# Optimization experiments

Measured on AMD Instinct MI355X. Metric: run time of the kernel, lower is better.

## Reference

```python
import math
import jax, jax.numpy as jnp
import numpy as np

B = 128          # batch_size (graphs)
SEQ = 128        # max_seq_len (nodes per graph)
D = 128          # input_dim
HID = 64         # enc_hidden_dim
HEADS = 4        # in_head
N = B * SEQ      # total nodes
E = 262144       # edges (avg degree 16)


def _make_pe(seq, d):
    pos = np.arange(seq, dtype=np.float32)[:, None]
    i_even = np.arange(0, d, 2, dtype=np.float32)
    pe = np.zeros((seq, d), dtype=np.float32)
    pe[:, 0::2] = np.sin(pos / 10000.0 ** (2.0 * i_even / d))
    pe[:, 1::2] = np.cos(pos / 10000.0 ** (2.0 * (i_even + 1.0) / d))
    return jnp.asarray(pe)


def setup_inputs() -> dict:
    key = jax.random.key(0)
    ks = jax.random.split(key, 10)
    s = 0.1
    return {
        "x": jax.random.normal(ks[0], (N, D), jnp.float32),
        "edge_index": jax.random.randint(ks[1], (2, E), 0, N),
        "pe": _make_pe(SEQ, D),
        "W1": jax.random.normal(ks[2], (D, HEADS * HID), jnp.float32) * s,
        "a_src1": jax.random.normal(ks[3], (HEADS, HID), jnp.float32) * s,
        "a_dst1": jax.random.normal(ks[4], (HEADS, HID), jnp.float32) * s,
        "b1": jnp.zeros((HEADS * HID,), jnp.float32),
        "W2": jax.random.normal(ks[5], (HEADS * HID, HID), jnp.float32) * s,
        "a_src2": jax.random.normal(ks[6], (1, HID), jnp.float32) * s,
        "a_dst2": jax.random.normal(ks[7], (1, HID), jnp.float32) * s,
        "b2": jnp.zeros((HID,), jnp.float32),
        "batch_size": B,
    }


def _gat_conv(x, src, dst, W, a_src, a_dst, b, heads, ch, concat, n):
    # PyG GATConv (eval mode, self-loops already appended to src/dst).
    h = (x @ W).reshape(n, heads, ch)                      # [N,H,C]
    alpha_src = jnp.einsum("nhc,hc->nh", h, a_src)         # [N,H]
    alpha_dst = jnp.einsum("nhc,hc->nh", h, a_dst)
    e = jax.nn.leaky_relu(alpha_src[src] + alpha_dst[dst], 0.2)  # [E,H]
    m = jax.ops.segment_max(e, dst, num_segments=n)        # segment softmax over dst
    ex = jnp.exp(e - m[dst])
    den = jax.ops.segment_sum(ex, dst, num_segments=n)
    alpha = ex / (den[dst] + 1e-16)                        # [E,H]
    out = jax.ops.segment_sum(h[src] * alpha[:, :, None], dst, num_segments=n)
    out = out.reshape(n, heads * ch) if concat else out.mean(axis=1)
    return out + b


def reference(x, edge_index, pe, W1, a_src1, a_dst1, b1, W2, a_src2, a_dst2, b2, batch_size):
    n = x.shape[0]
    loop = jnp.arange(n)
    src = jnp.concatenate([edge_index[0], loop])           # add self-loops (PyG default)
    dst = jnp.concatenate([edge_index[1], loop])
    # positional encoding (dropout inactive in eval)
    h = x * math.sqrt(x.shape[1]) + jnp.tile(pe, (batch_size, 1))
    h = jax.nn.elu(_gat_conv(h, src, dst, W1, a_src1, a_dst1, b1, HEADS, HID, True, n))
    out = _gat_conv(h, src, dst, W2, a_src2, a_dst2, b2, 1, HID, False, n)
    return out.reshape(batch_size, -1, out.shape[1])
```

## Files before the change

kernel.cpp:

```cpp
#include <hip/hip_runtime.h>
#include <hip/hip_bf16.h>

typedef __hip_bfloat16 bf16;
typedef __attribute__((ext_vector_type(8))) short short8v;
typedef __attribute__((ext_vector_type(4))) float f32x4;

#define N_NODES 16384
#define D_IN    128
#define HID     64
#define HEADS   4
#define F1      256
#define SEQ     128
#define SLOTS   64

__device__ __forceinline__ float wave_sum(float v) {
    #pragma unroll
    for (int o = 32; o > 0; o >>= 1) v += __shfl_xor(v, o, 64);
    return v;
}
__device__ __forceinline__ float lrelu(float v) { return v > 0.f ? v : 0.2f * v; }
__device__ __forceinline__ float bfu(unsigned short u) {
    return __uint_as_float((unsigned)u << 16);
}
__device__ __forceinline__ unsigned short f2b(float f) {
    unsigned u = __float_as_uint(f);
    return (unsigned short)((u + 0x7fffu + ((u >> 16) & 1u)) >> 16);
}

__global__ __launch_bounds__(256) void k_prep(const float* __restrict__ W1,
                                              const float* __restrict__ a_s1,
                                              const float* __restrict__ a_d1,
                                              unsigned short* __restrict__ w1hi,
                                              unsigned short* __restrict__ w1lo,
                                              float* __restrict__ gs,
                                              float* __restrict__ gd,
                                              int* __restrict__ cnt) {
    int gid = blockIdx.x * 256 + threadIdx.x;
    int j  = gid & 7;
    int l  = (gid >> 3) & 63;
    int ks = (gid >> 9) & 3;
    int n  = gid >> 11;
    int k   = ks * 32 + ((l >> 4) << 3) + j;
    int col = n * 16 + (l & 15);
    float w = W1[(size_t)k * 256 + col];
    unsigned short hi = f2b(w);
    w1hi[gid] = hi;
    w1lo[gid] = f2b(w - bfu(hi));
    if (gid < N_NODES) cnt[gid] = 0;
    if (gid < 512) {
        int kk = gid >> 2, hd = gid & 3;
        const float* wr = W1 + (size_t)kk * 256 + hd * 64;
        const float* as = a_s1 + hd * 64;
        const float* ad = a_d1 + hd * 64;
        float s = 0.f, d2 = 0.f;
        for (int c = 0; c < 64; c++) { float wv = wr[c]; s += wv * as[c]; d2 += wv * ad[c]; }
        gs[gid] = s; gd[gid] = d2;
    }
}

__global__ __launch_bounds__(256, 4) void k_gemm1m(const float* __restrict__ x,
                                                   const float* __restrict__ pe,
                                                   const unsigned short* __restrict__ w1hi,
                                                   const unsigned short* __restrict__ w1lo,
                                                   const float* __restrict__ gs,
                                                   const float* __restrict__ gd,
                                                   bf16* __restrict__ h,
                                                   float* __restrict__ as1,
                                                   float* __restrict__ ad1,
                                                   const int* __restrict__ ei, int E, int Etot,
                                                   int* __restrict__ cnt,
                                                   int* __restrict__ esrc) {
    int tid = threadIdx.x, lane = tid & 63, wv = tid >> 6;

    for (int e = blockIdx.x * 256 + tid; e < Etot; e += 131072) {
        int s, d;
        if (e < E) { s = ei[e]; d = ei[E + e]; }
        else       { s = e - E; d = s; }
        int pos = atomicAdd(&cnt[d], 1);
        if (pos < SLOTS) esrc[d * SLOTS + pos] = s;
    }

    int strip = blockIdx.x * 2 + (wv >> 1);
    int nhalf = wv & 1;
    int rowb = strip * 16;
    int r0 = lane & 15;
    int kg = lane >> 4;
    int kb = kg * 8;

    short8v afh[4], afl[4];
    f32x4 ls = {0.f, 0.f, 0.f, 0.f};
    f32x4 ld = {0.f, 0.f, 0.f, 0.f};
    #pragma unroll
    for (int ks = 0; ks < 4; ks++) {
        const float* xp = x  + (size_t)(rowb + r0) * 128 + ks * 32 + kb;
        const float* pp = pe + (size_t)((rowb + r0) & (SEQ - 1)) * 128 + ks * 32 + kb;
        float4 xa = *(const float4*)xp;
        float4 xb = *(const float4*)(xp + 4);
        float4 pa = *(const float4*)pp;
        float4 pb = *(const float4*)(pp + 4);
        float v[8];
        v[0] = xa.x * 11.313708499f + pa.x;
        v[1] = xa.y * 11.313708499f + pa.y;
        v[2] = xa.z * 11.313708499f + pa.z;
        v[3] = xa.w * 11.313708499f + pa.w;
        v[4] = xb.x * 11.313708499f + pb.x;
        v[5] = xb.y * 11.313708499f + pb.y;
        v[6] = xb.z * 11.313708499f + pb.z;
        v[7] = xb.w * 11.313708499f + pb.w;
        short8v ah, al;
        #pragma unroll
        for (int j = 0; j < 8; j++) {
            unsigned short hi = f2b(v[j]);
            ah[j] = (short)hi;
            al[j] = (short)f2b(v[j] - bfu(hi));
        }
        afh[ks] = ah; afl[ks] = al;
        if (nhalf == 0) {
            #pragma unroll
            for (int j = 0; j < 8; j++) {
                int k = ks * 32 + kb + j;
                float4 g4 = *(const float4*)(gs + k * 4);
                float4 h4 = *(const float4*)(gd + k * 4);
                ls.x += v[j] * g4.x; ls.y += v[j] * g4.y;
                ls.z += v[j] * g4.z; ls.w += v[j] * g4.w;
                ld.x += v[j] * h4.x; ld.y += v[j] * h4.y;
                ld.z += v[j] * h4.z; ld.w += v[j] * h4.w;
            }
        }
    }
    if (nhalf == 0) {
        #pragma unroll
        for (int o = 16; o < 64; o <<= 1) {
            ls.x += __shfl_xor(ls.x, o); ls.y += __shfl_xor(ls.y, o);
            ls.z += __shfl_xor(ls.z, o); ls.w += __shfl_xor(ls.w, o);
            ld.x += __shfl_xor(ld.x, o); ld.y += __shfl_xor(ld.y, o);
            ld.z += __shfl_xor(ld.z, o); ld.w += __shfl_xor(ld.w, o);
        }
        if (lane < 16) {
            int row = rowb + lane;
            *(float4*)(as1 + row * 4) = make_float4(ls.x, ls.y, ls.z, ls.w);
            *(float4*)(ad1 + row * 4) = make_float4(ld.x, ld.y, ld.z, ld.w);
        }
    }

    const short8v* wph = (const short8v*)w1hi;
    const short8v* wpl = (const short8v*)w1lo;
    unsigned short* hu = (unsigned short*)h;
    #pragma unroll
    for (int t = 0; t < 8; t++) {
        int n = nhalf * 8 + t;
        f32x4 acc = {0.f, 0.f, 0.f, 0.f};
        #pragma unroll
        for (int ks = 0; ks < 4; ks++) {
            short8v bh = wph[(n * 4 + ks) * 64 + lane];
            short8v bl = wpl[(n * 4 + ks) * 64 + lane];
            acc = __builtin_amdgcn_mfma_f32_16x16x32_bf16(afh[ks], bh, acc, 0, 0, 0);
            acc = __builtin_amdgcn_mfma_f32_16x16x32_bf16(afl[ks], bh, acc, 0, 0, 0);
            acc = __builtin_amdgcn_mfma_f32_16x16x32_bf16(afh[ks], bl, acc, 0, 0, 0);
        }
        #pragma unroll
        for (int r = 0; r < 4; r++)
            hu[(size_t)(rowb + kg * 4 + r) * 256 + n * 16 + r0] = f2b(acc[r]);
    }
}

__global__ __launch_bounds__(256) void k_agg1_gemm2(
        const int* __restrict__ cnt, const int* __restrict__ esrc,
        const float* __restrict__ as1, const float* __restrict__ ad1,
        const bf16* __restrict__ h,
        const float* __restrict__ b1,
        const float* __restrict__ W2,
        const float* __restrict__ a_src2, const float* __restrict__ a_dst2,
        bf16* __restrict__ h2, float* __restrict__ as2, float* __restrict__ ad2) {
    __shared__ float hs[4][256];
    __shared__ int2  st[4][4][64];
    int tid = threadIdx.x, lane = tid & 63, wv = tid >> 6;
    int dbase = blockIdx.x * 4;
    int d = dbase + wv;
    int deg = min(cnt[d], SLOTS);

    {
        int s = esrc[(size_t)d * SLOTS + lane] & (N_NODES - 1);
        float4 av = *(const float4*)(as1 + (size_t)s * 4);
        float4 dv = *(const float4*)(ad1 + (size_t)d * 4);
        bool live = lane < deg;
        float t0 = live ? __expf(lrelu(av.x + dv.x) - 40.f) : 0.f;
        float t1 = live ? __expf(lrelu(av.y + dv.y) - 40.f) : 0.f;
        float t2 = live ? __expf(lrelu(av.z + dv.z) - 40.f) : 0.f;
        float t3 = live ? __expf(lrelu(av.w + dv.w) - 40.f) : 0.f;
        float i0 = 1.f / wave_sum(t0);
        float i1 = 1.f / wave_sum(t1);
        float i2 = 1.f / wave_sum(t2);
        float i3 = 1.f / wave_sum(t3);
        int2 p0; p0.x = s; p0.y = __float_as_int(t0 * i0); st[wv][0][lane] = p0;
        int2 p1; p1.x = s; p1.y = __float_as_int(t1 * i1); st[wv][1][lane] = p1;
        int2 p2; p2.x = s; p2.y = __float_as_int(t2 * i2); st[wv][2][lane] = p2;
        int2 p3; p3.x = s; p3.y = __float_as_int(t3 * i3); st[wv][3][lane] = p3;
    }

    {
        int hd = lane >> 4;
        const int4* stp4 = (const int4*)st[wv][hd];
        const uint2* hb = (const uint2*)h;
        float a0 = 0.f, a1 = 0.f, a2 = 0.f, a3 = 0.f;
        int np = (deg + 1) >> 1;
        int4 P = stp4[0];
        uint2 u0 = hb[(size_t)P.x * 64 + lane];
        uint2 u1 = hb[(size_t)P.z * 64 + lane];
        for (int q = 1; q < np; q++) {
            int4 Pn = stp4[q];
            uint2 v0 = hb[(size_t)Pn.x * 64 + lane];
            uint2 v1 = hb[(size_t)Pn.z * 64 + lane];
            float ta = __uint_as_float(P.y), tb = __uint_as_float(P.w);
            a0 += __uint_as_float(u0.x << 16) * ta;
            a1 += __uint_as_float(u0.x & 0xffff0000u) * ta;
            a2 += __uint_as_float(u0.y << 16) * ta;
            a3 += __uint_as_float(u0.y & 0xffff0000u) * ta;
            a0 += __uint_as_float(u1.x << 16) * tb;
            a1 += __uint_as_float(u1.x & 0xffff0000u) * tb;
            a2 += __uint_as_float(u1.y << 16) * tb;
            a3 += __uint_as_float(u1.y & 0xffff0000u) * tb;
            P = Pn; u0 = v0; u1 = v1;
        }
        float ta = __uint_as_float(P.y), tb = __uint_as_float(P.w);
        a0 += __uint_as_float(u0.x << 16) * ta;
        a1 += __uint_as_float(u0.x & 0xffff0000u) * ta;
        a2 += __uint_as_float(u0.y << 16) * ta;
        a3 += __uint_as_float(u0.y & 0xffff0000u) * ta;
        a0 += __uint_as_float(u1.x << 16) * tb;
        a1 += __uint_as_float(u1.x & 0xffff0000u) * tb;
        a2 += __uint_as_float(u1.y << 16) * tb;
        a3 += __uint_as_float(u1.y & 0xffff0000u) * tb;

        float4 bb = *(const float4*)(b1 + lane * 4);
        float o0 = a0 + bb.x, o1 = a1 + bb.y, o2 = a2 + bb.z, o3 = a3 + bb.w;
        o0 = o0 > 0.f ? o0 : (__expf(o0) - 1.f);
        o1 = o1 > 0.f ? o1 : (__expf(o1) - 1.f);
        o2 = o2 > 0.f ? o2 : (__expf(o2) - 1.f);
        o3 = o3 > 0.f ? o3 : (__expf(o3) - 1.f);
        *(float4*)&hs[wv][lane * 4] = make_float4(o0, o1, o2, o3);
    }
    __syncthreads();

    float* part = (float*)st;

    {
        float acc2[4] = {0, 0, 0, 0};
        const int k4base = wv * 16;
        for (int kk = 0; kk < 16; kk++) {
            int k4 = k4base + kk;
            const float* wp = W2 + (size_t)k4 * 256 + lane;
            float w0 = wp[0], w1 = wp[64], w2 = wp[128], w3 = wp[192];
            #pragma unroll
            for (int r = 0; r < 4; r++) {
                float4 u = *(const float4*)&hs[r][k4 * 4];
                acc2[r] += u.x * w0 + u.y * w1 + u.z * w2 + u.w * w3;
            }
        }
        #pragma unroll
        for (int r = 0; r < 4; r++) part[(wv * 4 + r) * 64 + lane] = acc2[r];
    }
    __syncthreads();
    {
        int r = wv;
        float a0 = part[(0 * 4 + r) * 64 + lane] + part[(1 * 4 + r) * 64 + lane]
                 + part[(2 * 4 + r) * 64 + lane] + part[(3 * 4 + r) * 64 + lane];
        float asj = a_src2[lane], adj = a_dst2[lane];
        int n0 = dbase + r;
        h2[(size_t)n0 * 64 + lane] = __float2bfloat16(a0);
        float va0 = wave_sum(a0 * asj);
        float vd0 = wave_sum(a0 * adj);
        if (lane == 0) {
            as2[n0] = va0; ad2[n0] = vd0;
        }
    }
}

__global__ __launch_bounds__(256) void k_agg2(const int* __restrict__ cnt,
                                              const int* __restrict__ esrc,
                                              const float* __restrict__ as2,
                                              const float* __restrict__ ad2,
                                              const bf16* __restrict__ h2,
                                              const float* __restrict__ b2v,
                                              float* __restrict__ out) {
    __shared__ int2 sts2[4][64];
    int tid = threadIdx.x, lane = tid & 63, wv = tid >> 6;
    int d = blockIdx.x * 4 + wv;
    int deg = min(cnt[d], SLOTS);

    int s = esrc[(size_t)d * SLOTS + lane] & (N_NODES - 1);
    float av = as2[s];
    float adw = ad2[d];
    float t = (lane < deg) ? __expf(lrelu(av + adw) - 40.f) : 0.f;
    float inv = 1.f / wave_sum(t);
    int2 pr; pr.x = s; pr.y = __float_as_int(t * inv);
    sts2[wv][lane] = pr;

    const unsigned short* hb = (const unsigned short*)h2 + lane;
    const int4* row4 = (const int4*)sts2[wv];
    int nq = (deg + 3) >> 2;
    float acc = 0.f;
    int4 A = row4[0];
    int4 B = row4[1];
    unsigned short e0 = hb[(size_t)A.x * 64];
    unsigned short e1 = hb[(size_t)A.z * 64];
    unsigned short e2 = hb[(size_t)B.x * 64];
    unsigned short e3 = hb[(size_t)B.z * 64];
    for (int q = 1; q < nq; q++) {
        int4 An = row4[2 * q];
        int4 Bn = row4[2 * q + 1];
        unsigned short f0 = hb[(size_t)An.x * 64];
        unsigned short f1 = hb[(size_t)An.z * 64];
        unsigned short f2 = hb[(size_t)Bn.x * 64];
        unsigned short f3 = hb[(size_t)Bn.z * 64];
        acc += bfu(e0) * __uint_as_float(A.y);
        acc += bfu(e1) * __uint_as_float(A.w);
        acc += bfu(e2) * __uint_as_float(B.y);
        acc += bfu(e3) * __uint_as_float(B.w);
        A = An; B = Bn; e0 = f0; e1 = f1; e2 = f2; e3 = f3;
    }
    acc += bfu(e0) * __uint_as_float(A.y);
    acc += bfu(e1) * __uint_as_float(A.w);
    acc += bfu(e2) * __uint_as_float(B.y);
    acc += bfu(e3) * __uint_as_float(B.w);
    out[(size_t)d * 64 + lane] = acc + b2v[lane];
}

extern "C" void kernel_launch(void* const* d_in, const int* in_sizes, int n_in,
                              void* d_out, int out_size, void* d_ws, size_t ws_size,
                              hipStream_t stream) {
    const float* x    = (const float*)d_in[0];
    const int*   ei   = (const int*)  d_in[1];
    const float* pe   = (const float*)d_in[2];
    const float* W1   = (const float*)d_in[3];
    const float* a_s1 = (const float*)d_in[4];
    const float* a_d1 = (const float*)d_in[5];
    const float* b1   = (const float*)d_in[6];
    const float* W2   = (const float*)d_in[7];
    const float* a_s2 = (const float*)d_in[8];
    const float* a_d2 = (const float*)d_in[9];
    const float* b2   = (const float*)d_in[10];

    const int E    = in_sizes[1] / 2;
    const int n    = N_NODES;
    const int Etot = E + n;

    char* p = (char*)d_ws;
    auto alloc = [&](size_t bytes) -> void* {
        void* r = (void*)p;
        p += (bytes + 255) & ~(size_t)255;
        return r;
    };
    int*   cnt     = (int*)  alloc((size_t)n * 4);
    int*   esrc    = (int*)  alloc((size_t)n * SLOTS * 4);
    bf16*  h       = (bf16*) alloc((size_t)n * F1 * 2);
    float* as1     = (float*)alloc((size_t)n * HEADS * 4);
    float* ad1     = (float*)alloc((size_t)n * HEADS * 4);
    bf16*  h2      = (bf16*) alloc((size_t)n * HID * 2);
    float* as2     = (float*)alloc((size_t)n * 4);
    float* ad2     = (float*)alloc((size_t)n * 4);
    unsigned short* w1hi = (unsigned short*)alloc((size_t)D_IN * F1 * 2);
    unsigned short* w1lo = (unsigned short*)alloc((size_t)D_IN * F1 * 2);
    float* gs      = (float*)alloc((size_t)D_IN * HEADS * 4);
    float* gd      = (float*)alloc((size_t)D_IN * HEADS * 4);

    k_prep      <<<128, 256, 0, stream>>>(W1, a_s1, a_d1, w1hi, w1lo, gs, gd, cnt);
    k_gemm1m    <<<n / 32, 256, 0, stream>>>(x, pe, w1hi, w1lo, gs, gd, h, as1, ad1,
                                             ei, E, Etot, cnt, esrc);
    k_agg1_gemm2<<<n / 4, 256, 0, stream>>>(cnt, esrc, as1, ad1, h, b1,
                                            W2, a_s2, a_d2, h2, as2, ad2);
    k_agg2      <<<n / 4, 256, 0, stream>>>(cnt, esrc, as2, ad2, h2, b2, (float*)d_out);
}
```

Measured before the change: 155.2 us.

## Split gemm1 output columns across four waves and vectorize agg2 gathers

The first GEMM kernel now gives each block a single 16-row strip, with each of the four waves computing four of the sixteen output column tiles. This doubles the grid to raise parallelism, and the edge-insertion loop stride is doubled to match. The layer-2 aggregation now has each wave handle four edges at once, with 16 lanes per edge loading 8-byte chunks of the bf16 row. The partial sums are then reduced across lane groups with shuffles, replacing the scalar 2-byte per-lane gathers. The cost is redundant x/pe loading and conversion per wave in gemm1, plus extra shuffle reductions in agg2.

```diff
diff --git a/kernel.cpp b/kernel.cpp
--- a/kernel.cpp
+++ b/kernel.cpp
@@ -72,7 +72,7 @@
                                                    int* __restrict__ esrc) {
     int tid = threadIdx.x, lane = tid & 63, wv = tid >> 6;
 
-    for (int e = blockIdx.x * 256 + tid; e < Etot; e += 131072) {
+    for (int e = blockIdx.x * 256 + tid; e < Etot; e += 262144) {
         int s, d;
         if (e < E) { s = ei[e]; d = ei[E + e]; }
         else       { s = e - E; d = s; }
@@ -80,9 +80,7 @@
         if (pos < SLOTS) esrc[d * SLOTS + pos] = s;
     }
 
-    int strip = blockIdx.x * 2 + (wv >> 1);
-    int nhalf = wv & 1;
-    int rowb = strip * 16;
+    int rowb = blockIdx.x * 16;
     int r0 = lane & 15;
     int kg = lane >> 4;
     int kb = kg * 8;
@@ -115,7 +113,7 @@
             al[j] = (short)f2b(v[j] - bfu(hi));
         }
         afh[ks] = ah; afl[ks] = al;
-        if (nhalf == 0) {
+        if (wv == 0) {
             #pragma unroll
             for (int j = 0; j < 8; j++) {
                 int k = ks * 32 + kb + j;
@@ -128,7 +126,7 @@
             }
         }
     }
-    if (nhalf == 0) {
+    if (wv == 0) {
         #pragma unroll
         for (int o = 16; o < 64; o <<= 1) {
             ls.x += __shfl_xor(ls.x, o); ls.y += __shfl_xor(ls.y, o);
@@ -147,8 +145,8 @@
     const short8v* wpl = (const short8v*)w1lo;
     unsigned short* hu = (unsigned short*)h;
     #pragma unroll
-    for (int t = 0; t < 8; t++) {
-        int n = nhalf * 8 + t;
+    for (int t = 0; t < 4; t++) {
+        int n = wv * 4 + t;
         f32x4 acc = {0.f, 0.f, 0.f, 0.f};
         #pragma unroll
         for (int ks = 0; ks < 4; ks++) {
@@ -288,42 +286,52 @@
     int d = blockIdx.x * 4 + wv;
     int deg = min(cnt[d], SLOTS);
 
-    int s = esrc[(size_t)d * SLOTS + lane] & (N_NODES - 1);
-    float av = as2[s];
-    float adw = ad2[d];
-    float t = (lane < deg) ? __expf(lrelu(av + adw) - 40.f) : 0.f;
-    float inv = 1.f / wave_sum(t);
-    int2 pr; pr.x = s; pr.y = __float_as_int(t * inv);
-    sts2[wv][lane] = pr;
-
-    const unsigned short* hb = (const unsigned short*)h2 + lane;
-    const int4* row4 = (const int4*)sts2[wv];
+    {
+        int s = esrc[(size_t)d * SLOTS + lane] & (N_NODES - 1);
+        float av = as2[s];
+        float adw = ad2[d];
+        float t = (lane < deg) ? __expf(lrelu(av + adw) - 40.f) : 0.f;
+        float inv = 1.f / wave_sum(t);
+        int2 pr; pr.x = s; pr.y = __float_as_int(t * inv);
+        sts2[wv][lane] = pr;
+    }
+
+    int g = lane >> 4;
+    int c16 = lane & 15;
+    const uint2* hb2 = (const uint2*)h2;
+    float a0 = 0.f, a1 = 0.f, a2 = 0.f, a3 = 0.f;
     int nq = (deg + 3) >> 2;
-    float acc = 0.f;
-    int4 A = row4[0];
-    int4 B = row4[1];
-    unsigned short e0 = hb[(size_t)A.x * 64];
-    unsigned short e1 = hb[(size_t)A.z * 64];
-    unsigned short e2 = hb[(size_t)B.x * 64];
-    unsigned short e3 = hb[(size_t)B.z * 64];
+    int2 P = sts2[wv][g];
+    uint2 u = hb2[(size_t)P.x * 16 + c16];
     for (int q = 1; q < nq; q++) {
-        int4 An = row4[2 * q];
-        int4 Bn = row4[2 * q + 1];
-        unsigned short f0 = hb[(size_t)An.x * 64];
-        unsigned short f1 = hb[(size_t)An.z * 64];
-        unsigned short f2 = hb[(size_t)Bn.x * 64];
-        unsigned short f3 = hb[(size_t)Bn.z * 64];
-        acc += bfu(e0) * __uint_as_float(A.y);
-        acc += bfu(e1) * __uint_as_float(A.w);
-        acc += bfu(e2) * __uint_as_float(B.y);
-        acc += bfu(e3) * __uint_as_float(B.w);
-        A = An; B = Bn; e0 = f0; e1 = f1; e2 = f2; e3 = f3;
-    }
-    acc += bfu(e0) * __uint_as_float(A.y);
-    acc += bfu(e1) * __uint_as_float(A.w);
-    acc += bfu(e2) * __uint_as_float(B.y);
-    acc += bfu(e3) * __uint_as_float(B.w);
-    out[(size_t)d * 64 + lane] = acc + b2v[lane];
+        int2 Pn = sts2[wv][4 * q + g];
+        uint2 un = hb2[(size_t)Pn.x * 16 + c16];
+        float t = __int_as_float(P.y);
+        a0 += __uint_as_float(u.x << 16) * t;
+        a1 += __uint_as_float(u.x & 0xffff0000u) * t;
+        a2 += __uint_as_float(u.y << 16) * t;
+        a3 += __uint_as_float(u.y & 0xffff0000u) * t;
+        P = Pn; u = un;
+    }
+    {
+        float t = __int_as_float(P.y);
+        a0 += __uint_as_float(u.x << 16) * t;
+        a1 += __uint_as_float(u.x & 0xffff0000u) * t;
+        a2 += __uint_as_float(u.y << 16) * t;
+        a3 += __uint_as_float(u.y & 0xffff0000u) * t;
+    }
+    #pragma unroll
+    for (int o = 16; o < 64; o <<= 1) {
+        a0 += __shfl_xor(a0, o);
+        a1 += __shfl_xor(a1, o);
+        a2 += __shfl_xor(a2, o);
+        a3 += __shfl_xor(a3, o);
+    }
+    if (lane < 16) {
+        float4 bb = *(const float4*)(b2v + c16 * 4);
+        float4* dst = (float4*)(out + (size_t)d * 64 + c16 * 4);
+        *dst = make_float4(a0 + bb.x, a1 + bb.y, a2 + bb.z, a3 + bb.w);
+    }
 }
 
 extern "C" void kernel_launch(void* const* d_in, const int* in_sizes, int n_in,
@@ -365,7 +373,7 @@
     float* gd      = (float*)alloc((size_t)D_IN * HEADS * 4);
 
     k_prep      <<<128, 256, 0, stream>>>(W1, a_s1, a_d1, w1hi, w1lo, gs, gd, cnt);
-    k_gemm1m    <<<n / 32, 256, 0, stream>>>(x, pe, w1hi, w1lo, gs, gd, h, as1, ad1,
+    k_gemm1m    <<<n / 16, 256, 0, stream>>>(x, pe, w1hi, w1lo, gs, gd, h, as1, ad1,
                                              ei, E, Etot, cnt, esrc);
     k_agg1_gemm2<<<n / 4, 256, 0, stream>>>(cnt, esrc, as1, ad1, h, b1,
                                             W2, a_s2, a_d2, h2, as2, ad2);
```

New measurement: 154.8 us. About the same (-0.3%).
